# Kernel tuning notes

Hardware: AMD Instinct MI355X
Metric: run time of the kernel (lower is better)

## Reference

```python
import jax, jax.numpy as jnp
import numpy as np

N = 100000
E = 1600000
F = 128
H = 128
EPS = 1e-5
NEG_SLOPE = 0.2


def setup_inputs() -> dict:
    key = jax.random.key(0)
    ks = jax.random.split(key, 24)
    def nrm(k, shape, scale=0.05):
        return jax.random.normal(k, shape, dtype=jnp.float32) * scale
    inp = {
        'x': jax.random.normal(ks[0], (N, F), dtype=jnp.float32),
        'edge_index': jax.random.randint(ks[1], (2, E), 0, N, dtype=jnp.int64),
        # conv 0: F -> H
        'W0': nrm(ks[2], (F, H)), 'asrc0': nrm(ks[3], (H,)), 'adst0': nrm(ks[4], (H,)), 'b0': nrm(ks[5], (H,)),
        # convs 1..4 (middle): H -> H, stacked
        'Wm': nrm(ks[6], (4, H, H)), 'asrcm': nrm(ks[7], (4, H)), 'adstm': nrm(ks[8], (4, H)), 'bm': nrm(ks[9], (4, H)),
        # conv 5 (last): H -> H
        'W5': nrm(ks[10], (H, H)), 'asrc5': nrm(ks[11], (H,)), 'adst5': nrm(ks[12], (H,)), 'b5': nrm(ks[13], (H,)),
        # batchnorm affine params for all 6 layers
        'gammas': jnp.ones((6, H), dtype=jnp.float32), 'betas': jnp.zeros((6, H), dtype=jnp.float32),
        # residual transform F -> H and output layer H -> F
        'Wr': nrm(ks[14], (F, H)), 'br': nrm(ks[15], (H,)),
        'Wo': nrm(ks[16], (H, F)), 'bo': nrm(ks[17], (F,)),
    }
    return inp


def _gat_layer(x, W, a_src, a_dst, b, src, dst):
    # PyG GATConv, heads=1: h = x W; e_ij = LeakyReLU(a_src.h_j + a_dst.h_i)
    # softmax over incoming edges of each destination node, scatter-add aggregate.
    h = x @ W                              # [N, H]
    s = h @ a_src                          # [N]
    d = h @ a_dst                          # [N]
    e = jax.nn.leaky_relu(s[src] + d[dst], NEG_SLOPE)   # [E']
    m = jax.ops.segment_max(e, dst, num_segments=N)      # per-dst max (self-loops guarantee nonempty)
    p = jnp.exp(e - m[dst])
    z = jax.ops.segment_sum(p, dst, num_segments=N)
    alpha = p / z[dst]                     # [E']
    out = jax.ops.segment_sum(alpha[:, None] * h[src], dst, num_segments=N)
    return out + b


def _bn(x, g, beta):
    # BatchNorm1d, training mode (batch statistics, biased variance)
    mu = x.mean(axis=0)
    var = x.var(axis=0)
    return g * (x - mu) * jax.lax.rsqrt(var + EPS) + beta


def reference(x, edge_index, W0, asrc0, adst0, b0, Wm, asrcm, adstm, bm,
              W5, asrc5, adst5, b5, gammas, betas, Wr, br, Wo, bo):
    # add self-loops (PyG GATConv default)
    loops = jnp.arange(N, dtype=edge_index.dtype)
    src = jnp.concatenate([edge_index[0], loops])
    dst = jnp.concatenate([edge_index[1], loops])

    residual = x @ Wr + br
    # first 5 convs: conv -> bn -> relu -> (dropout=identity) -> +residual
    layer_params = [(W0, asrc0, adst0, b0)] + [
        (Wm[i], asrcm[i], adstm[i], bm[i]) for i in range(4)
    ]
    h = x
    for i, (W, a_s, a_d, b) in enumerate(layer_params):
        h = _gat_layer(h, W, a_s, a_d, b, src, dst)
        h = jax.nn.relu(_bn(h, gammas[i], betas[i]))
        h = h + residual
        residual = h
    # last conv -> bn -> out_layer
    h = _gat_layer(h, W5, asrc5, adst5, b5, src, dst)
    h = _bn(h, gammas[5], betas[5])
    return h @ Wo + bo
```

## Files before the change

kernel.cpp:

```cpp
#include <hip/hip_runtime.h>

#define NF 128
#define EPS 1e-5f
#define SLOPE 0.2f

typedef __attribute__((ext_vector_type(8))) short bf16x8;
typedef __attribute__((ext_vector_type(4))) float f32x4;

static __device__ __forceinline__ unsigned short f2bf(float f) {
  unsigned int u = __builtin_bit_cast(unsigned int, f);
  u += 0x7fffu + ((u >> 16) & 1u);
  return (unsigned short)(u >> 16);
}
static __device__ __forceinline__ float bf2f(unsigned short s) {
  return __builtin_bit_cast(float, (unsigned int)s << 16);
}
static __device__ __forceinline__ float bflo(unsigned int u) {
  return __builtin_bit_cast(float, u << 16);
}
static __device__ __forceinline__ float bfhi(unsigned int u) {
  return __builtin_bit_cast(float, u & 0xffff0000u);
}
static __device__ __forceinline__ unsigned int pack2(float a, float b) {
  return (unsigned int)f2bf(a) | ((unsigned int)f2bf(b) << 16);
}


__global__ void k_init_counts(int* counts, int n) {
  int i = blockIdx.x * 256 + threadIdx.x;
  if (i < n) counts[i] = 1;
}

__global__ void k_count(const int* __restrict__ dst, int* __restrict__ counts,
                        int* __restrict__ pos, int e) {
  int i = blockIdx.x * 256 + threadIdx.x;
  if (i < e) pos[i] = atomicAdd(&counts[dst[i]], 1);
}

__global__ void k_scan_part(const int* __restrict__ counts, int* __restrict__ partials, int n) {
  __shared__ int sd[256];
  int base = blockIdx.x * 2048;
  int sum = 0;
  for (int i = threadIdx.x; i < 2048; i += 256) {
    int idx = base + i;
    sum += (idx < n) ? counts[idx] : 0;
  }
  sd[threadIdx.x] = sum;
  __syncthreads();
  for (int s = 128; s > 0; s >>= 1) {
    if (threadIdx.x < s) sd[threadIdx.x] += sd[threadIdx.x + s];
    __syncthreads();
  }
  if (threadIdx.x == 0) partials[blockIdx.x] = sd[0];
}

__global__ void k_scan_mid(int* partials, int nb) {
  if (threadIdx.x == 0 && blockIdx.x == 0) {
    int acc = 0;
    for (int b = 0; b < nb; b++) { int v = partials[b]; partials[b] = acc; acc += v; }
  }
}

__global__ void k_scan_final(const int* __restrict__ counts, const int* __restrict__ partials,
                             int* __restrict__ offsets, int n) {
  __shared__ int sd[256];
  int t = threadIdx.x;
  int base = blockIdx.x * 2048;
  int local[8];
  int sum = 0;
#pragma unroll
  for (int j = 0; j < 8; j++) {
    int idx = base + t * 8 + j;
    int v = (idx < n) ? counts[idx] : 0;
    local[j] = sum;
    sum += v;
  }
  sd[t] = sum;
  __syncthreads();
  for (int st = 1; st < 256; st <<= 1) {
    int v = 0;
    if (t >= st) v = sd[t - st];
    __syncthreads();
    if (t >= st) sd[t] += v;
    __syncthreads();
  }
  int tb = partials[blockIdx.x] + (t > 0 ? sd[t - 1] : 0);
#pragma unroll
  for (int j = 0; j < 8; j++) {
    int idx = base + t * 8 + j;
    if (idx < n) offsets[idx] = tb + local[j];
  }
}

__global__ void k_selfloop(int* __restrict__ offsets, int* __restrict__ csr, int n, int total) {
  int i = blockIdx.x * 256 + threadIdx.x;
  if (i < n) csr[offsets[i]] = i;
  if (i == 0) offsets[n] = total;
}

__global__ void k_fill_pass(const int* __restrict__ src, const int* __restrict__ dst,
                            const int* __restrict__ offsets, const int* __restrict__ pos,
                            int* __restrict__ csr, int e, int lo, int hi) {
  int i = blockIdx.x * 256 + threadIdx.x;
  if (i < e) {
    int d = dst[i];
    if (d >= lo && d < hi) csr[offsets[d] + pos[i]] = src[i];
  }
}


__global__ void k_f32_to_bf16(const float* __restrict__ x, unsigned short* __restrict__ o,
                              int n, int np) {
  int i = blockIdx.x * 256 + threadIdx.x;
  if (i >= np * (NF / 4)) return;
  int row = i >> 5;
  ushort4 ov;
  if (row < n) {
    float4 v = ((const float4*)x)[i];
    ov = make_ushort4(f2bf(v.x), f2bf(v.y), f2bf(v.z), f2bf(v.w));
  } else {
    ov = make_ushort4(0, 0, 0, 0);
  }
  ((ushort4*)o)[i] = ov;
}

__global__ void k_wt(const float* __restrict__ W0, const float* __restrict__ Wm,
                     const float* __restrict__ W5, const float* __restrict__ Wr,
                     const float* __restrict__ Wo, unsigned short* __restrict__ Wt) {
  int idx = blockIdx.x * 256 + threadIdx.x;
  if (idx >= 8 * NF * NF) return;
  int mat = idx >> 14;
  int rem = idx & 16383;
  int r = rem >> 7;
  int k = rem & 127;
  const float* W = (mat == 0) ? W0
                 : (mat <= 4) ? Wm + (size_t)(mat - 1) * NF * NF
                 : (mat == 5) ? W5
                 : (mat == 6) ? Wr : Wo;
  Wt[idx] = f2bf(W[k * NF + r]);
}


template <int MODE>
__global__ __launch_bounds__(256) void k_gemm_mfma(
    const unsigned short* __restrict__ A, const unsigned short* __restrict__ Wt,
    const float* __restrict__ asrc, const float* __restrict__ adst,
    const float* __restrict__ bias, unsigned short* __restrict__ Cb,
    float* __restrict__ Cf, float* __restrict__ sv, float* __restrict__ dv, int n,
    const unsigned short* __restrict__ agg, const unsigned short* __restrict__ res,
    const float* __restrict__ scsh, unsigned short* __restrict__ hout) {
  int w = threadIdx.x >> 6;
  int l = threadIdx.x & 63;
  int lr = l & 15, lh = l >> 4;
  int row0 = blockIdx.x * 128 + w * 32;

  bf16x8 af[2][4];
  if (MODE <= 2) {
    const unsigned short* Ab = A + (size_t)(row0 + lr) * NF + lh * 8;
#pragma unroll
    for (int m = 0; m < 2; m++)
#pragma unroll
      for (int kk = 0; kk < 4; kk++)
        af[m][kk] = *(const bf16x8*)(Ab + m * 16 * NF + kk * 32);
  } else {
#pragma unroll
    for (int kk = 0; kk < 4; kk++) {
      int c0 = lh * 8 + kk * 32;
      float4 scA = *(const float4*)&scsh[c0];
      float4 scB = *(const float4*)&scsh[c0 + 4];
      float4 shA = *(const float4*)&scsh[128 + c0];
      float4 shB = *(const float4*)&scsh[128 + c0 + 4];
#pragma unroll
      for (int m = 0; m < 2; m++) {
        size_t base = (size_t)(row0 + lr + m * 16) * NF + c0;
        uint4 ag = *(const uint4*)(agg + base);
        float v0 = bflo(ag.x) * scA.x + shA.x;
        float v1 = bfhi(ag.x) * scA.y + shA.y;
        float v2 = bflo(ag.y) * scA.z + shA.z;
        float v3 = bfhi(ag.y) * scA.w + shA.w;
        float v4 = bflo(ag.z) * scB.x + shB.x;
        float v5 = bfhi(ag.z) * scB.y + shB.y;
        float v6 = bflo(ag.w) * scB.z + shB.z;
        float v7 = bfhi(ag.w) * scB.w + shB.w;
        if (MODE == 3) {
          uint4 rs = *(const uint4*)(res + base);
          v0 = fmaxf(v0, 0.f) + bflo(rs.x);
          v1 = fmaxf(v1, 0.f) + bfhi(rs.x);
          v2 = fmaxf(v2, 0.f) + bflo(rs.y);
          v3 = fmaxf(v3, 0.f) + bfhi(rs.y);
          v4 = fmaxf(v4, 0.f) + bflo(rs.z);
          v5 = fmaxf(v5, 0.f) + bfhi(rs.z);
          v6 = fmaxf(v6, 0.f) + bflo(rs.w);
          v7 = fmaxf(v7, 0.f) + bfhi(rs.w);
        }
        uint4 hv;
        hv.x = pack2(v0, v1);
        hv.y = pack2(v2, v3);
        hv.z = pack2(v4, v5);
        hv.w = pack2(v6, v7);
        if (MODE == 3) *(uint4*)(hout + base) = hv;
        af[m][kk] = __builtin_bit_cast(bf16x8, hv);
      }
    }
  }

  f32x4 acc[2][8];
#pragma unroll
  for (int m = 0; m < 2; m++)
#pragma unroll
    for (int nn = 0; nn < 8; nn++) acc[m][nn] = (f32x4){0.f, 0.f, 0.f, 0.f};

  const unsigned short* Bb = Wt + (size_t)lr * NF + lh * 8;
#pragma unroll
  for (int kk = 0; kk < 4; kk++) {
    bf16x8 bfr[8];
#pragma unroll
    for (int nn = 0; nn < 8; nn++)
      bfr[nn] = *(const bf16x8*)(Bb + nn * 16 * NF + kk * 32);
#pragma unroll
    for (int m = 0; m < 2; m++)
#pragma unroll
      for (int nn = 0; nn < 8; nn++)
        acc[m][nn] = __builtin_amdgcn_mfma_f32_16x16x32_bf16(af[m][kk], bfr[nn], acc[m][nn], 0, 0, 0);
  }

  if (MODE == 0 || MODE == 3) {
    float as[8], ad[8];
#pragma unroll
    for (int nn = 0; nn < 8; nn++) {
      as[nn] = asrc[nn * 16 + lr];
      ad[nn] = adst[nn * 16 + lr];
    }
#pragma unroll
    for (int m = 0; m < 2; m++) {
#pragma unroll
      for (int r = 0; r < 4; r++) {
        int row = row0 + m * 16 + lh * 4 + r;
        float sp = 0.f, dp = 0.f;
#pragma unroll
        for (int nn = 0; nn < 8; nn++) {
          float v = acc[m][nn][r];
          sp += v * as[nn];
          dp += v * ad[nn];
          Cb[(size_t)row * NF + nn * 16 + lr] = f2bf(v);
        }
#pragma unroll
        for (int mk = 8; mk > 0; mk >>= 1) {
          sp += __shfl_xor(sp, mk);
          dp += __shfl_xor(dp, mk);
        }
        if (lr == 0) { sv[row] = sp; dv[row] = dp; }
      }
    }
  } else if (MODE == 1 || MODE == 4) {
    float bcol[8];
#pragma unroll
    for (int nn = 0; nn < 8; nn++) bcol[nn] = bias[nn * 16 + lr];
#pragma unroll
    for (int m = 0; m < 2; m++)
#pragma unroll
      for (int r = 0; r < 4; r++) {
        int row = row0 + m * 16 + lh * 4 + r;
        if (row < n) {
#pragma unroll
          for (int nn = 0; nn < 8; nn++)
            Cf[(size_t)row * NF + nn * 16 + lr] = acc[m][nn][r] + bcol[nn];
        }
      }
  } else {
    float bcol[8];
#pragma unroll
    for (int nn = 0; nn < 8; nn++) bcol[nn] = bias[nn * 16 + lr];
#pragma unroll
    for (int m = 0; m < 2; m++)
#pragma unroll
      for (int r = 0; r < 4; r++) {
        int row = row0 + m * 16 + lh * 4 + r;
#pragma unroll
        for (int nn = 0; nn < 8; nn++)
          Cb[(size_t)row * NF + nn * 16 + lr] = f2bf(acc[m][nn][r] + bcol[nn]);
      }
  }
}


__global__ __launch_bounds__(256) void k_attn_gather(
    const float* __restrict__ sv, const float* __restrict__ dv,
    const int* __restrict__ offs, const int* __restrict__ csr,
    const unsigned short* __restrict__ hbf, const float* __restrict__ bias,
    unsigned short* __restrict__ aggb, float* __restrict__ pstat, int n) {
  int w = threadIdx.x >> 6, l = threadIdx.x & 63;
  int ll = l & 15, g = l >> 4;
  int node0 = blockIdx.x * 16 + w * 4;
  float ps[8] = {0.f, 0.f, 0.f, 0.f, 0.f, 0.f, 0.f, 0.f};
  float qs[8] = {0.f, 0.f, 0.f, 0.f, 0.f, 0.f, 0.f, 0.f};
  float4 bv0 = *(const float4*)&bias[8 * ll];
  float4 bv1 = *(const float4*)&bias[8 * ll + 4];

  __shared__ uint2 s_pair[4][72];

  for (int ni = 0; ni < 4; ni++) {
    int node = node0 + ni;
    if (node >= n) break;
    int o0 = offs[node], o1 = offs[node + 1];
    int deg = o1 - o0;
    float di = dv[node];
    float a[8] = {0.f, 0.f, 0.f, 0.f, 0.f, 0.f, 0.f, 0.f};

    if (deg <= 64) {
      bool valid = l < deg;
      int srcj = valid ? csr[o0 + l] : 0;
      float ev = valid ? sv[srcj] + di : -1e30f;
      ev = ev >= 0.f ? ev : SLOPE * ev;
      float m = ev;
#pragma unroll
      for (int k2 = 32; k2 > 0; k2 >>= 1) m = fmaxf(m, __shfl_xor(m, k2));
      float pe = valid ? __expf(ev - m) : 0.f;
      float z = pe;
#pragma unroll
      for (int k2 = 32; k2 > 0; k2 >>= 1) z += __shfl_xor(z, k2);
      float wj = pe / z;

      s_pair[w][l] = make_uint2((unsigned)srcj, __builtin_bit_cast(unsigned, wj));
      if (l < 8) s_pair[w][64 + l] = make_uint2(0u, 0u);

      for (int j = g; j < deg; j += 8) {
        uint2 pA = s_pair[w][j];
        uint2 pB = s_pair[w][j + 4];
        int sA = (int)pA.x, sB = (int)pB.x;
        float wA = __builtin_bit_cast(float, pA.y);
        float wB = __builtin_bit_cast(float, pB.y);
        uint4 hA = *(const uint4*)(hbf + (size_t)sA * NF + 8 * ll);
        uint4 hB = *(const uint4*)(hbf + (size_t)sB * NF + 8 * ll);
        a[0] += wA * bflo(hA.x) + wB * bflo(hB.x);
        a[1] += wA * bfhi(hA.x) + wB * bfhi(hB.x);
        a[2] += wA * bflo(hA.y) + wB * bflo(hB.y);
        a[3] += wA * bfhi(hA.y) + wB * bfhi(hB.y);
        a[4] += wA * bflo(hA.z) + wB * bflo(hB.z);
        a[5] += wA * bfhi(hA.z) + wB * bfhi(hB.z);
        a[6] += wA * bflo(hA.w) + wB * bflo(hB.w);
        a[7] += wA * bfhi(hA.w) + wB * bfhi(hB.w);
      }
    } else {
      float m = -1e30f;
      for (int j = o0 + l; j < o1; j += 64) {
        float ev = sv[csr[j]] + di;
        ev = ev >= 0.f ? ev : SLOPE * ev;
        m = fmaxf(m, ev);
      }
#pragma unroll
      for (int k2 = 32; k2 > 0; k2 >>= 1) m = fmaxf(m, __shfl_xor(m, k2));
      float z = 0.f;
      for (int j = o0 + l; j < o1; j += 64) {
        float ev = sv[csr[j]] + di;
        ev = ev >= 0.f ? ev : SLOPE * ev;
        z += __expf(ev - m);
      }
#pragma unroll
      for (int k2 = 32; k2 > 0; k2 >>= 1) z += __shfl_xor(z, k2);
      float inv = 1.f / z;
      for (int t2 = 0; t2 < deg; t2 += 4) {
        int tt = t2 + g;
        if (tt < deg) {
          int sI = csr[o0 + tt];
          float ev = sv[sI] + di;
          ev = ev >= 0.f ? ev : SLOPE * ev;
          float wI = __expf(ev - m) * inv;
          uint4 hv = *(const uint4*)(hbf + (size_t)sI * NF + 8 * ll);
          a[0] += wI * bflo(hv.x);
          a[1] += wI * bfhi(hv.x);
          a[2] += wI * bflo(hv.y);
          a[3] += wI * bfhi(hv.y);
          a[4] += wI * bflo(hv.z);
          a[5] += wI * bfhi(hv.z);
          a[6] += wI * bflo(hv.w);
          a[7] += wI * bfhi(hv.w);
        }
      }
    }
#pragma unroll
    for (int j = 0; j < 8; j++) {
      a[j] += __shfl_xor(a[j], 16);
      a[j] += __shfl_xor(a[j], 32);
    }
    if (g == 0) {
      a[0] += bv0.x; a[1] += bv0.y; a[2] += bv0.z; a[3] += bv0.w;
      a[4] += bv1.x; a[5] += bv1.y; a[6] += bv1.z; a[7] += bv1.w;
      uint4 ov;
      ov.x = pack2(a[0], a[1]);
      ov.y = pack2(a[2], a[3]);
      ov.z = pack2(a[4], a[5]);
      ov.w = pack2(a[6], a[7]);
      *(uint4*)(aggb + (size_t)node * NF + 8 * ll) = ov;
#pragma unroll
      for (int j = 0; j < 8; j++) { ps[j] += a[j]; qs[j] += a[j] * a[j]; }
    }
  }

  __shared__ float red[4][16][17];
  if (g == 0) {
#pragma unroll
    for (int j = 0; j < 8; j++) {
      red[w][ll][j] = ps[j];
      red[w][ll][8 + j] = qs[j];
    }
  }
  __syncthreads();
  int t = threadIdx.x;
  int c = t & 127, kind = t >> 7;
  int li = c >> 3, sj = (c & 7) + 8 * kind;
  float v = red[0][li][sj] + red[1][li][sj] + red[2][li][sj] + red[3][li][sj];
  atomicAdd(&pstat[(blockIdx.x & 63) * 256 + t], v);
}


__global__ void k_bnfinal(float* __restrict__ pstat, const float* __restrict__ gamma,
                          const float* __restrict__ beta, float* __restrict__ scsh,
                          float ninv) {
  __shared__ float tot[256];
  int t = threadIdx.x;
  float v = 0.f;
  for (int s2 = 0; s2 < 64; s2++) {
    v += pstat[s2 * 256 + t];
    pstat[s2 * 256 + t] = 0.f;
  }
  tot[t] = v;
  __syncthreads();
  if (t < 128) {
    float mu = tot[t] * ninv;
    float var = tot[128 + t] * ninv - mu * mu;
    float sc = gamma[t] * rsqrtf(var + EPS);
    scsh[t] = sc;
    scsh[128 + t] = beta[t] - mu * sc;
  }
}


extern "C" void kernel_launch(void* const* d_in, const int* in_sizes, int n_in,
                              void* d_out, int out_size, void* d_ws, size_t ws_size,
                              hipStream_t stream) {
  (void)n_in; (void)out_size; (void)ws_size;
  const float* x     = (const float*)d_in[0];
  const int*   ei    = (const int*)d_in[1];
  const float* W0    = (const float*)d_in[2];
  const float* asrc0 = (const float*)d_in[3];
  const float* adst0 = (const float*)d_in[4];
  const float* b0    = (const float*)d_in[5];
  const float* Wm    = (const float*)d_in[6];
  const float* asrcm = (const float*)d_in[7];
  const float* adstm = (const float*)d_in[8];
  const float* bm    = (const float*)d_in[9];
  const float* W5    = (const float*)d_in[10];
  const float* asrc5 = (const float*)d_in[11];
  const float* adst5 = (const float*)d_in[12];
  const float* b5    = (const float*)d_in[13];
  const float* gammas= (const float*)d_in[14];
  const float* betas = (const float*)d_in[15];
  const float* Wr    = (const float*)d_in[16];
  const float* br    = (const float*)d_in[17];
  const float* Wo    = (const float*)d_in[18];
  const float* bo    = (const float*)d_in[19];

  const int n = in_sizes[0] / NF;
  const int np = (n + 127) & ~127;
  const int e = in_sizes[1] / 2;
  const int tot = e + n;
  const int* srcp = ei;
  const int* dstp = ei + e;

  char* w = (char*)d_ws;
  auto carve = [&](size_t bytes) {
    char* p = w;
    w += (bytes + 255) & ~(size_t)255;
    return p;
  };
  unsigned short* h_bf    = (unsigned short*)carve((size_t)np * NF * 2);
  unsigned short* hlin_bf = (unsigned short*)carve((size_t)np * NF * 2);
  unsigned short* res_bf  = (unsigned short*)carve((size_t)np * NF * 2);
  unsigned short* agg_bf  = (unsigned short*)carve((size_t)np * NF * 2);
  unsigned short* Wt      = (unsigned short*)carve((size_t)8 * NF * NF * 2);
  float* sv      = (float*)carve((size_t)np * 4);
  float* dv      = (float*)carve((size_t)np * 4);
  int*   csr     = (int*)carve((size_t)tot * 4);
  int*   offsets = (int*)carve((size_t)(n + 1) * 4);
  int*   counts  = (int*)carve((size_t)n * 4);
  int*   pos     = (int*)carve((size_t)e * 4);
  int*   partials= (int*)carve(64 * 4);
  float* pstat   = (float*)carve(64 * 256 * 4);
  float* scsh    = (float*)carve(256 * 4);

  int nb = (n + 2047) / 2048;

  k_wt<<<(8 * NF * NF + 255) / 256, 256, 0, stream>>>(W0, Wm, W5, Wr, Wo, Wt);
  k_f32_to_bf16<<<(np * (NF / 4) + 255) / 256, 256, 0, stream>>>(x, h_bf, n, np);

  k_init_counts<<<(n + 255) / 256, 256, 0, stream>>>(counts, n);
  k_count<<<(e + 255) / 256, 256, 0, stream>>>(dstp, counts, pos, e);
  k_scan_part<<<nb, 256, 0, stream>>>(counts, partials, n);
  k_scan_mid<<<1, 64, 0, stream>>>(partials, nb);
  k_scan_final<<<nb, 256, 0, stream>>>(counts, partials, offsets, n);
  k_selfloop<<<(n + 255) / 256, 256, 0, stream>>>(offsets, csr, n, tot);
  {
    const int NPASS = 8;
    int step = (n + NPASS - 1) / NPASS;
    for (int p = 0; p < NPASS; p++) {
      int lo = p * step;
      int hi = min(n, lo + step);
      k_fill_pass<<<(e + 255) / 256, 256, 0, stream>>>(srcp, dstp, offsets, pos, csr, e, lo, hi);
    }
  }

  hipMemsetAsync(pstat, 0, 64 * 256 * 4, stream);

  int gemm_grid = np / 128;

  k_gemm_mfma<2><<<gemm_grid, 256, 0, stream>>>(h_bf, Wt + 6 * NF * NF, nullptr, nullptr,
                                                br, res_bf, nullptr, nullptr, nullptr, n,
                                                nullptr, nullptr, nullptr, nullptr);

  for (int L = 0; L < 6; L++) {
    const float *als, *ald, *bl;
    if (L == 0)      { als = asrc0; ald = adst0; bl = b0; }
    else if (L <= 4) { als = asrcm + (L - 1) * NF; ald = adstm + (L - 1) * NF; bl = bm + (L - 1) * NF; }
    else             { als = asrc5; ald = adst5; bl = b5; }

    if (L == 0) {
      k_gemm_mfma<0><<<gemm_grid, 256, 0, stream>>>(h_bf, Wt, als, ald, nullptr, hlin_bf,
                                                    nullptr, sv, dv, n,
                                                    nullptr, nullptr, nullptr, nullptr);
    } else {
      const unsigned short* resb = (L == 1) ? res_bf : h_bf;
      k_gemm_mfma<3><<<gemm_grid, 256, 0, stream>>>(nullptr, Wt + (size_t)L * NF * NF,
                                                    als, ald, nullptr, hlin_bf, nullptr, sv, dv, n,
                                                    agg_bf, resb, scsh, h_bf);
    }

    k_attn_gather<<<(n + 15) / 16, 256, 0, stream>>>(sv, dv, offsets, csr, hlin_bf, bl,
                                                     agg_bf, pstat, n);
    k_bnfinal<<<1, 256, 0, stream>>>(pstat, gammas + L * NF, betas + L * NF, scsh, 1.0f / n);
  }

  k_gemm_mfma<4><<<gemm_grid, 256, 0, stream>>>(nullptr, Wt + 7 * NF * NF, nullptr, nullptr,
                                                bo, nullptr, (float*)d_out, nullptr, nullptr, n,
                                                agg_bf, nullptr, scsh, nullptr);
}
```

Before: 890.5 us.

## Split attention into alpha pass and feature-sliced gather over column-sliced h

```diff
diff --git a/kernel.cpp b/kernel.cpp
--- a/kernel.cpp
+++ b/kernel.cpp
@@ -11,9 +11,6 @@
   unsigned int u = __builtin_bit_cast(unsigned int, f);
   u += 0x7fffu + ((u >> 16) & 1u);
   return (unsigned short)(u >> 16);
-}
-static __device__ __forceinline__ float bf2f(unsigned short s) {
-  return __builtin_bit_cast(float, (unsigned int)s << 16);
 }
 static __device__ __forceinline__ float bflo(unsigned int u) {
   return __builtin_bit_cast(float, u << 16);
@@ -153,6 +150,7 @@
   int l = threadIdx.x & 63;
   int lr = l & 15, lh = l >> 4;
   int row0 = blockIdx.x * 128 + w * 32;
+  size_t sstr = (size_t)gridDim.x * 128 * 16;
 
   bf16x8 af[2][4];
   if (MODE <= 2) {
@@ -242,7 +240,7 @@
           float v = acc[m][nn][r];
           sp += v * as[nn];
           dp += v * ad[nn];
-          Cb[(size_t)row * NF + nn * 16 + lr] = f2bf(v);
+          Cb[(size_t)nn * sstr + (size_t)row * 16 + lr] = f2bf(v);
         }
 #pragma unroll
         for (int mk = 8; mk > 0; mk >>= 1) {
@@ -284,29 +282,18 @@
 }
 
 
-__global__ __launch_bounds__(256) void k_attn_gather(
+__global__ __launch_bounds__(256) void k_alpha(
     const float* __restrict__ sv, const float* __restrict__ dv,
     const int* __restrict__ offs, const int* __restrict__ csr,
-    const unsigned short* __restrict__ hbf, const float* __restrict__ bias,
-    unsigned short* __restrict__ aggb, float* __restrict__ pstat, int n) {
+    unsigned int* __restrict__ packed, int n) {
   int w = threadIdx.x >> 6, l = threadIdx.x & 63;
-  int ll = l & 15, g = l >> 4;
   int node0 = blockIdx.x * 16 + w * 4;
-  float ps[8] = {0.f, 0.f, 0.f, 0.f, 0.f, 0.f, 0.f, 0.f};
-  float qs[8] = {0.f, 0.f, 0.f, 0.f, 0.f, 0.f, 0.f, 0.f};
-  float4 bv0 = *(const float4*)&bias[8 * ll];
-  float4 bv1 = *(const float4*)&bias[8 * ll + 4];
-
-  __shared__ uint2 s_pair[4][72];
-
   for (int ni = 0; ni < 4; ni++) {
     int node = node0 + ni;
     if (node >= n) break;
     int o0 = offs[node], o1 = offs[node + 1];
     int deg = o1 - o0;
     float di = dv[node];
-    float a[8] = {0.f, 0.f, 0.f, 0.f, 0.f, 0.f, 0.f, 0.f};
-
     if (deg <= 64) {
       bool valid = l < deg;
       int srcj = valid ? csr[o0 + l] : 0;
@@ -320,26 +307,9 @@
 #pragma unroll
       for (int k2 = 32; k2 > 0; k2 >>= 1) z += __shfl_xor(z, k2);
       float wj = pe / z;
-
-      s_pair[w][l] = make_uint2((unsigned)srcj, __builtin_bit_cast(unsigned, wj));
-      if (l < 8) s_pair[w][64 + l] = make_uint2(0u, 0u);
-
-      for (int j = g; j < deg; j += 8) {
-        uint2 pA = s_pair[w][j];
-        uint2 pB = s_pair[w][j + 4];
-        int sA = (int)pA.x, sB = (int)pB.x;
-        float wA = __builtin_bit_cast(float, pA.y);
-        float wB = __builtin_bit_cast(float, pB.y);
-        uint4 hA = *(const uint4*)(hbf + (size_t)sA * NF + 8 * ll);
-        uint4 hB = *(const uint4*)(hbf + (size_t)sB * NF + 8 * ll);
-        a[0] += wA * bflo(hA.x) + wB * bflo(hB.x);
-        a[1] += wA * bfhi(hA.x) + wB * bfhi(hB.x);
-        a[2] += wA * bflo(hA.y) + wB * bflo(hB.y);
-        a[3] += wA * bfhi(hA.y) + wB * bfhi(hB.y);
-        a[4] += wA * bflo(hA.z) + wB * bflo(hB.z);
-        a[5] += wA * bfhi(hA.z) + wB * bfhi(hB.z);
-        a[6] += wA * bflo(hA.w) + wB * bflo(hB.w);
-        a[7] += wA * bfhi(hA.w) + wB * bfhi(hB.w);
+      if (valid) {
+        unsigned q = (unsigned)(wj * 32767.f + 0.5f);
+        packed[o0 + l] = ((unsigned)srcj << 15) | q;
       }
     } else {
       float m = -1e30f;
@@ -359,58 +329,84 @@
 #pragma unroll
       for (int k2 = 32; k2 > 0; k2 >>= 1) z += __shfl_xor(z, k2);
       float inv = 1.f / z;
-      for (int t2 = 0; t2 < deg; t2 += 4) {
-        int tt = t2 + g;
-        if (tt < deg) {
-          int sI = csr[o0 + tt];
-          float ev = sv[sI] + di;
-          ev = ev >= 0.f ? ev : SLOPE * ev;
-          float wI = __expf(ev - m) * inv;
-          uint4 hv = *(const uint4*)(hbf + (size_t)sI * NF + 8 * ll);
-          a[0] += wI * bflo(hv.x);
-          a[1] += wI * bfhi(hv.x);
-          a[2] += wI * bflo(hv.y);
-          a[3] += wI * bfhi(hv.y);
-          a[4] += wI * bflo(hv.z);
-          a[5] += wI * bfhi(hv.z);
-          a[6] += wI * bflo(hv.w);
-          a[7] += wI * bfhi(hv.w);
-        }
-      }
-    }
-#pragma unroll
-    for (int j = 0; j < 8; j++) {
-      a[j] += __shfl_xor(a[j], 16);
-      a[j] += __shfl_xor(a[j], 32);
-    }
-    if (g == 0) {
-      a[0] += bv0.x; a[1] += bv0.y; a[2] += bv0.z; a[3] += bv0.w;
-      a[4] += bv1.x; a[5] += bv1.y; a[6] += bv1.z; a[7] += bv1.w;
-      uint4 ov;
-      ov.x = pack2(a[0], a[1]);
-      ov.y = pack2(a[2], a[3]);
-      ov.z = pack2(a[4], a[5]);
-      ov.w = pack2(a[6], a[7]);
-      *(uint4*)(aggb + (size_t)node * NF + 8 * ll) = ov;
-#pragma unroll
-      for (int j = 0; j < 8; j++) { ps[j] += a[j]; qs[j] += a[j] * a[j]; }
-    }
-  }
-
-  __shared__ float red[4][16][17];
-  if (g == 0) {
-#pragma unroll
-    for (int j = 0; j < 8; j++) {
-      red[w][ll][j] = ps[j];
-      red[w][ll][8 + j] = qs[j];
-    }
+      for (int j = o0 + l; j < o1; j += 64) {
+        int sI = csr[j];
+        float ev = sv[sI] + di;
+        ev = ev >= 0.f ? ev : SLOPE * ev;
+        float wj = __expf(ev - m) * inv;
+        unsigned q = (unsigned)(wj * 32767.f + 0.5f);
+        packed[j] = ((unsigned)sI << 15) | q;
+      }
+    }
+  }
+}
+
+
+__global__ __launch_bounds__(256) void k_gather_slice(
+    const unsigned int* __restrict__ packed, const int* __restrict__ offs,
+    const unsigned short* __restrict__ hs, const float* __restrict__ bias,
+    unsigned short* __restrict__ aggb, float* __restrict__ pstat, int n, int np) {
+  int slice = blockIdx.x & 7;
+  int chunk = blockIdx.x >> 3;
+  int th = threadIdx.x;
+  int w2 = th >> 6, l = th & 63;
+  int h2 = l >> 5, lh2 = l & 31;
+  int e = lh2 >> 2, c = lh2 & 3;
+  const unsigned short* hsl = hs + (size_t)slice * np * 16 + c * 4;
+  float4 bv = *(const float4*)&bias[slice * 16 + c * 4];
+  float ps0 = 0.f, ps1 = 0.f, ps2 = 0.f, ps3 = 0.f;
+  float qs0 = 0.f, qs1 = 0.f, qs2 = 0.f, qs3 = 0.f;
+
+  for (int r = 0; r < 8; r++) {
+    int node = chunk * 64 + r * 8 + w2 * 2 + h2;
+    float a0 = 0.f, a1 = 0.f, a2 = 0.f, a3 = 0.f;
+    if (node < n) {
+      int o0 = offs[node], o1 = offs[node + 1];
+      for (int j = o0 + e; j < o1; j += 8) {
+        unsigned u = packed[j];
+        float al = (float)(u & 32767u) * (1.f / 32767.f);
+        uint2 hv = *(const uint2*)(hsl + (size_t)(u >> 15) * 16);
+        a0 += al * bflo(hv.x);
+        a1 += al * bfhi(hv.x);
+        a2 += al * bflo(hv.y);
+        a3 += al * bfhi(hv.y);
+      }
+    }
+#pragma unroll
+    for (int mk = 4; mk <= 16; mk <<= 1) {
+      a0 += __shfl_xor(a0, mk);
+      a1 += __shfl_xor(a1, mk);
+      a2 += __shfl_xor(a2, mk);
+      a3 += __shfl_xor(a3, mk);
+    }
+    if (e == 0 && node < n) {
+      a0 += bv.x; a1 += bv.y; a2 += bv.z; a3 += bv.w;
+      *(uint2*)(aggb + (size_t)node * NF + slice * 16 + c * 4) =
+          make_uint2(pack2(a0, a1), pack2(a2, a3));
+      ps0 += a0; qs0 += a0 * a0;
+      ps1 += a1; qs1 += a1 * a1;
+      ps2 += a2; qs2 += a2 * a2;
+      ps3 += a3; qs3 += a3 * a3;
+    }
+  }
+
+  __shared__ float sred[8][4][4], qred[8][4][4];
+  if (e == 0) {
+    int who = w2 * 2 + h2;
+    sred[who][c][0] = ps0; sred[who][c][1] = ps1;
+    sred[who][c][2] = ps2; sred[who][c][3] = ps3;
+    qred[who][c][0] = qs0; qred[who][c][1] = qs1;
+    qred[who][c][2] = qs2; qred[who][c][3] = qs3;
   }
   __syncthreads();
-  int t = threadIdx.x;
-  int c = t & 127, kind = t >> 7;
-  int li = c >> 3, sj = (c & 7) + 8 * kind;
-  float v = red[0][li][sj] + red[1][li][sj] + red[2][li][sj] + red[3][li][sj];
-  atomicAdd(&pstat[(blockIdx.x & 63) * 256 + t], v);
+  if (th < 32) {
+    int kind = th >> 4, lc = th & 15;
+    float s = 0.f;
+#pragma unroll
+    for (int i = 0; i < 8; i++)
+      s += kind ? qred[i][lc >> 2][lc & 3] : sred[i][lc >> 2][lc & 3];
+    atomicAdd(&pstat[(size_t)((blockIdx.x >> 3) & 63) * 256 + kind * 128 + slice * 16 + lc], s);
+  }
 }
 
 
@@ -475,13 +471,14 @@
     return p;
   };
   unsigned short* h_bf    = (unsigned short*)carve((size_t)np * NF * 2);
-  unsigned short* hlin_bf = (unsigned short*)carve((size_t)np * NF * 2);
+  unsigned short* hs      = (unsigned short*)carve((size_t)np * NF * 2);
   unsigned short* res_bf  = (unsigned short*)carve((size_t)np * NF * 2);
   unsigned short* agg_bf  = (unsigned short*)carve((size_t)np * NF * 2);
   unsigned short* Wt      = (unsigned short*)carve((size_t)8 * NF * NF * 2);
   float* sv      = (float*)carve((size_t)np * 4);
   float* dv      = (float*)carve((size_t)np * 4);
   int*   csr     = (int*)carve((size_t)tot * 4);
+  unsigned int* packed = (unsigned int*)carve((size_t)tot * 4);
   int*   offsets = (int*)carve((size_t)(n + 1) * 4);
   int*   counts  = (int*)carve((size_t)n * 4);
   int*   pos     = (int*)carve((size_t)e * 4);
@@ -513,6 +510,7 @@
   hipMemsetAsync(pstat, 0, 64 * 256 * 4, stream);
 
   int gemm_grid = np / 128;
+  int gs_grid = ((n + 63) / 64) * 8;
 
   k_gemm_mfma<2><<<gemm_grid, 256, 0, stream>>>(h_bf, Wt + 6 * NF * NF, nullptr, nullptr,
                                                 br, res_bf, nullptr, nullptr, nullptr, n,
@@ -525,18 +523,18 @@
     else             { als = asrc5; ald = adst5; bl = b5; }
 
     if (L == 0) {
-      k_gemm_mfma<0><<<gemm_grid, 256, 0, stream>>>(h_bf, Wt, als, ald, nullptr, hlin_bf,
+      k_gemm_mfma<0><<<gemm_grid, 256, 0, stream>>>(h_bf, Wt, als, ald, nullptr, hs,
                                                     nullptr, sv, dv, n,
                                                     nullptr, nullptr, nullptr, nullptr);
     } else {
       const unsigned short* resb = (L == 1) ? res_bf : h_bf;
       k_gemm_mfma<3><<<gemm_grid, 256, 0, stream>>>(nullptr, Wt + (size_t)L * NF * NF,
-                                                    als, ald, nullptr, hlin_bf, nullptr, sv, dv, n,
+                                                    als, ald, nullptr, hs, nullptr, sv, dv, n,
                                                     agg_bf, resb, scsh, h_bf);
     }
 
-    k_attn_gather<<<(n + 15) / 16, 256, 0, stream>>>(sv, dv, offsets, csr, hlin_bf, bl,
-                                                     agg_bf, pstat, n);
+    k_alpha<<<(n + 15) / 16, 256, 0, stream>>>(sv, dv, offsets, csr, packed, n);
+    k_gather_slice<<<gs_grid, 256, 0, stream>>>(packed, offsets, hs, bl, agg_bf, pstat, n, np);
     k_bnfinal<<<1, 256, 0, stream>>>(pstat, gammas + L * NF, betas + L * NF, scsh, 1.0f / n);
   }
 
```

Measured after the change: 1.351 ms. 51.7% more time.

## Build CSR with per-node atomic cursors and skip unused residual store in last layer

Applied to the files above, without the earlier changes.

```diff
diff --git a/kernel.cpp b/kernel.cpp
--- a/kernel.cpp
+++ b/kernel.cpp
@@ -12,9 +12,6 @@
   u += 0x7fffu + ((u >> 16) & 1u);
   return (unsigned short)(u >> 16);
 }
-static __device__ __forceinline__ float bf2f(unsigned short s) {
-  return __builtin_bit_cast(float, (unsigned int)s << 16);
-}
 static __device__ __forceinline__ float bflo(unsigned int u) {
   return __builtin_bit_cast(float, u << 16);
 }
@@ -31,10 +28,9 @@
   if (i < n) counts[i] = 1;
 }
 
-__global__ void k_count(const int* __restrict__ dst, int* __restrict__ counts,
-                        int* __restrict__ pos, int e) {
+__global__ void k_count(const int* __restrict__ dst, int* __restrict__ counts, int e) {
   int i = blockIdx.x * 256 + threadIdx.x;
-  if (i < e) pos[i] = atomicAdd(&counts[dst[i]], 1);
+  if (i < e) atomicAdd(&counts[dst[i]], 1);
 }
 
 __global__ void k_scan_part(const int* __restrict__ counts, int* __restrict__ partials, int n) {
@@ -92,19 +88,27 @@
   }
 }
 
-__global__ void k_selfloop(int* __restrict__ offsets, int* __restrict__ csr, int n, int total) {
+__global__ void k_selfloop(int* __restrict__ offsets, int* __restrict__ cursor,
+                           int* __restrict__ csr, int n, int total) {
   int i = blockIdx.x * 256 + threadIdx.x;
-  if (i < n) csr[offsets[i]] = i;
+  if (i < n) {
+    int o = offsets[i];
+    csr[o] = i;
+    cursor[i] = o + 1;
+  }
   if (i == 0) offsets[n] = total;
 }
 
 __global__ void k_fill_pass(const int* __restrict__ src, const int* __restrict__ dst,
-                            const int* __restrict__ offsets, const int* __restrict__ pos,
-                            int* __restrict__ csr, int e, int lo, int hi) {
+                            int* __restrict__ cursor, int* __restrict__ csr,
+                            int e, int lo, int hi) {
   int i = blockIdx.x * 256 + threadIdx.x;
   if (i < e) {
     int d = dst[i];
-    if (d >= lo && d < hi) csr[offsets[d] + pos[i]] = src[i];
+    if (d >= lo && d < hi) {
+      int p = atomicAdd(&cursor[d], 1);
+      csr[p] = src[i];
+    }
   }
 }
 
@@ -198,7 +202,7 @@
         hv.y = pack2(v2, v3);
         hv.z = pack2(v4, v5);
         hv.w = pack2(v6, v7);
-        if (MODE == 3) *(uint4*)(hout + base) = hv;
+        if (MODE == 3 && hout) *(uint4*)(hout + base) = hv;
         af[m][kk] = __builtin_bit_cast(bf16x8, hv);
       }
     }
@@ -484,7 +488,7 @@
   int*   csr     = (int*)carve((size_t)tot * 4);
   int*   offsets = (int*)carve((size_t)(n + 1) * 4);
   int*   counts  = (int*)carve((size_t)n * 4);
-  int*   pos     = (int*)carve((size_t)e * 4);
+  int*   cursor  = (int*)carve((size_t)n * 4);
   int*   partials= (int*)carve(64 * 4);
   float* pstat   = (float*)carve(64 * 256 * 4);
   float* scsh    = (float*)carve(256 * 4);
@@ -495,18 +499,18 @@
   k_f32_to_bf16<<<(np * (NF / 4) + 255) / 256, 256, 0, stream>>>(x, h_bf, n, np);
 
   k_init_counts<<<(n + 255) / 256, 256, 0, stream>>>(counts, n);
-  k_count<<<(e + 255) / 256, 256, 0, stream>>>(dstp, counts, pos, e);
+  k_count<<<(e + 255) / 256, 256, 0, stream>>>(dstp, counts, e);
   k_scan_part<<<nb, 256, 0, stream>>>(counts, partials, n);
   k_scan_mid<<<1, 64, 0, stream>>>(partials, nb);
   k_scan_final<<<nb, 256, 0, stream>>>(counts, partials, offsets, n);
-  k_selfloop<<<(n + 255) / 256, 256, 0, stream>>>(offsets, csr, n, tot);
+  k_selfloop<<<(n + 255) / 256, 256, 0, stream>>>(offsets, cursor, csr, n, tot);
   {
-    const int NPASS = 8;
+    const int NPASS = 4;
     int step = (n + NPASS - 1) / NPASS;
     for (int p = 0; p < NPASS; p++) {
       int lo = p * step;
       int hi = min(n, lo + step);
-      k_fill_pass<<<(e + 255) / 256, 256, 0, stream>>>(srcp, dstp, offsets, pos, csr, e, lo, hi);
+      k_fill_pass<<<(e + 255) / 256, 256, 0, stream>>>(srcp, dstp, cursor, csr, e, lo, hi);
     }
   }
 
@@ -530,9 +534,10 @@
                                                     nullptr, nullptr, nullptr, nullptr);
     } else {
       const unsigned short* resb = (L == 1) ? res_bf : h_bf;
+      unsigned short* houtp = (L < 5) ? h_bf : nullptr;
       k_gemm_mfma<3><<<gemm_grid, 256, 0, stream>>>(nullptr, Wt + (size_t)L * NF * NF,
                                                     als, ald, nullptr, hlin_bf, nullptr, sv, dv, n,
-                                                    agg_bf, resb, scsh, h_bf);
+                                                    agg_bf, resb, scsh, houtp);
     }
 
     k_attn_gather<<<(n + 15) / 16, 256, 0, stream>>>(sv, dv, offsets, csr, hlin_bf, bl,
```

Result: slower. 943.6 us (+6.0%).

## Split attention gather across column halves, single-pass CSR fill, skip unused h write

Applied to the files above, without the earlier changes.

```diff
diff --git a/kernel.cpp b/kernel.cpp
--- a/kernel.cpp
+++ b/kernel.cpp
@@ -11,9 +11,6 @@
   unsigned int u = __builtin_bit_cast(unsigned int, f);
   u += 0x7fffu + ((u >> 16) & 1u);
   return (unsigned short)(u >> 16);
-}
-static __device__ __forceinline__ float bf2f(unsigned short s) {
-  return __builtin_bit_cast(float, (unsigned int)s << 16);
 }
 static __device__ __forceinline__ float bflo(unsigned int u) {
   return __builtin_bit_cast(float, u << 16);
@@ -98,14 +95,11 @@
   if (i == 0) offsets[n] = total;
 }
 
-__global__ void k_fill_pass(const int* __restrict__ src, const int* __restrict__ dst,
-                            const int* __restrict__ offsets, const int* __restrict__ pos,
-                            int* __restrict__ csr, int e, int lo, int hi) {
+__global__ void k_fill(const int* __restrict__ src, const int* __restrict__ dst,
+                       const int* __restrict__ offsets, const int* __restrict__ pos,
+                       int* __restrict__ csr, int e) {
   int i = blockIdx.x * 256 + threadIdx.x;
-  if (i < e) {
-    int d = dst[i];
-    if (d >= lo && d < hi) csr[offsets[d] + pos[i]] = src[i];
-  }
+  if (i < e) csr[offsets[dst[i]] + pos[i]] = src[i];
 }
 
 
@@ -198,7 +192,7 @@
         hv.y = pack2(v2, v3);
         hv.z = pack2(v4, v5);
         hv.w = pack2(v6, v7);
-        if (MODE == 3) *(uint4*)(hout + base) = hv;
+        if (MODE == 3 && hout) *(uint4*)(hout + base) = hv;
         af[m][kk] = __builtin_bit_cast(bf16x8, hv);
       }
     }
@@ -290,14 +284,18 @@
     const unsigned short* __restrict__ hbf, const float* __restrict__ bias,
     unsigned short* __restrict__ aggb, float* __restrict__ pstat, int n) {
   int w = threadIdx.x >> 6, l = threadIdx.x & 63;
-  int ll = l & 15, g = l >> 4;
-  int node0 = blockIdx.x * 16 + w * 4;
+  int half = blockIdx.x & 1;
+  int chunk = blockIdx.x >> 1;
+  int e8 = l >> 3, c8 = l & 7;
+  int colbase = half * 64 + c8 * 8;
+  int node0 = chunk * 16 + w * 4;
   float ps[8] = {0.f, 0.f, 0.f, 0.f, 0.f, 0.f, 0.f, 0.f};
   float qs[8] = {0.f, 0.f, 0.f, 0.f, 0.f, 0.f, 0.f, 0.f};
-  float4 bv0 = *(const float4*)&bias[8 * ll];
-  float4 bv1 = *(const float4*)&bias[8 * ll + 4];
-
-  __shared__ uint2 s_pair[4][72];
+  float4 bv0 = *(const float4*)&bias[colbase];
+  float4 bv1 = *(const float4*)&bias[colbase + 4];
+
+  __shared__ uint2 s_pair[4][80];
+  if (l < 16) s_pair[w][64 + l] = make_uint2(0u, 0u);
 
   for (int ni = 0; ni < 4; ni++) {
     int node = node0 + ni;
@@ -322,16 +320,14 @@
       float wj = pe / z;
 
       s_pair[w][l] = make_uint2((unsigned)srcj, __builtin_bit_cast(unsigned, wj));
-      if (l < 8) s_pair[w][64 + l] = make_uint2(0u, 0u);
-
-      for (int j = g; j < deg; j += 8) {
+
+      for (int j = e8; j < deg; j += 16) {
         uint2 pA = s_pair[w][j];
-        uint2 pB = s_pair[w][j + 4];
-        int sA = (int)pA.x, sB = (int)pB.x;
+        uint2 pB = s_pair[w][j + 8];
         float wA = __builtin_bit_cast(float, pA.y);
         float wB = __builtin_bit_cast(float, pB.y);
-        uint4 hA = *(const uint4*)(hbf + (size_t)sA * NF + 8 * ll);
-        uint4 hB = *(const uint4*)(hbf + (size_t)sB * NF + 8 * ll);
+        uint4 hA = *(const uint4*)(hbf + (size_t)pA.x * NF + colbase);
+        uint4 hB = *(const uint4*)(hbf + (size_t)pB.x * NF + colbase);
         a[0] += wA * bflo(hA.x) + wB * bflo(hB.x);
         a[1] += wA * bfhi(hA.x) + wB * bfhi(hB.x);
         a[2] += wA * bflo(hA.y) + wB * bflo(hB.y);
@@ -359,31 +355,29 @@
 #pragma unroll
       for (int k2 = 32; k2 > 0; k2 >>= 1) z += __shfl_xor(z, k2);
       float inv = 1.f / z;
-      for (int t2 = 0; t2 < deg; t2 += 4) {
-        int tt = t2 + g;
-        if (tt < deg) {
-          int sI = csr[o0 + tt];
-          float ev = sv[sI] + di;
-          ev = ev >= 0.f ? ev : SLOPE * ev;
-          float wI = __expf(ev - m) * inv;
-          uint4 hv = *(const uint4*)(hbf + (size_t)sI * NF + 8 * ll);
-          a[0] += wI * bflo(hv.x);
-          a[1] += wI * bfhi(hv.x);
-          a[2] += wI * bflo(hv.y);
-          a[3] += wI * bfhi(hv.y);
-          a[4] += wI * bflo(hv.z);
-          a[5] += wI * bfhi(hv.z);
-          a[6] += wI * bflo(hv.w);
-          a[7] += wI * bfhi(hv.w);
-        }
+      for (int tt = o0 + e8; tt < o1; tt += 8) {
+        int sI = csr[tt];
+        float ev = sv[sI] + di;
+        ev = ev >= 0.f ? ev : SLOPE * ev;
+        float wI = __expf(ev - m) * inv;
+        uint4 hv = *(const uint4*)(hbf + (size_t)sI * NF + colbase);
+        a[0] += wI * bflo(hv.x);
+        a[1] += wI * bfhi(hv.x);
+        a[2] += wI * bflo(hv.y);
+        a[3] += wI * bfhi(hv.y);
+        a[4] += wI * bflo(hv.z);
+        a[5] += wI * bfhi(hv.z);
+        a[6] += wI * bflo(hv.w);
+        a[7] += wI * bfhi(hv.w);
       }
     }
 #pragma unroll
     for (int j = 0; j < 8; j++) {
+      a[j] += __shfl_xor(a[j], 8);
       a[j] += __shfl_xor(a[j], 16);
       a[j] += __shfl_xor(a[j], 32);
     }
-    if (g == 0) {
+    if (e8 == 0) {
       a[0] += bv0.x; a[1] += bv0.y; a[2] += bv0.z; a[3] += bv0.w;
       a[4] += bv1.x; a[5] += bv1.y; a[6] += bv1.z; a[7] += bv1.w;
       uint4 ov;
@@ -391,26 +385,29 @@
       ov.y = pack2(a[2], a[3]);
       ov.z = pack2(a[4], a[5]);
       ov.w = pack2(a[6], a[7]);
-      *(uint4*)(aggb + (size_t)node * NF + 8 * ll) = ov;
+      *(uint4*)(aggb + (size_t)node * NF + colbase) = ov;
 #pragma unroll
       for (int j = 0; j < 8; j++) { ps[j] += a[j]; qs[j] += a[j] * a[j]; }
     }
   }
 
-  __shared__ float red[4][16][17];
-  if (g == 0) {
+  __shared__ float red[4][8][17];
+  if (e8 == 0) {
 #pragma unroll
     for (int j = 0; j < 8; j++) {
-      red[w][ll][j] = ps[j];
-      red[w][ll][8 + j] = qs[j];
+      red[w][c8][j] = ps[j];
+      red[w][c8][8 + j] = qs[j];
     }
   }
   __syncthreads();
   int t = threadIdx.x;
-  int c = t & 127, kind = t >> 7;
-  int li = c >> 3, sj = (c & 7) + 8 * kind;
-  float v = red[0][li][sj] + red[1][li][sj] + red[2][li][sj] + red[3][li][sj];
-  atomicAdd(&pstat[(blockIdx.x & 63) * 256 + t], v);
+  if (t < 128) {
+    int kind = t >> 6;
+    int cc = t & 63;
+    int ci = cc >> 3, ck = (cc & 7) + 8 * kind;
+    float v = red[0][ci][ck] + red[1][ci][ck] + red[2][ci][ck] + red[3][ci][ck];
+    atomicAdd(&pstat[((blockIdx.x >> 1) & 63) * 256 + kind * 128 + half * 64 + cc], v);
+  }
 }
 
 
@@ -500,19 +497,12 @@
   k_scan_mid<<<1, 64, 0, stream>>>(partials, nb);
   k_scan_final<<<nb, 256, 0, stream>>>(counts, partials, offsets, n);
   k_selfloop<<<(n + 255) / 256, 256, 0, stream>>>(offsets, csr, n, tot);
-  {
-    const int NPASS = 8;
-    int step = (n + NPASS - 1) / NPASS;
-    for (int p = 0; p < NPASS; p++) {
-      int lo = p * step;
-      int hi = min(n, lo + step);
-      k_fill_pass<<<(e + 255) / 256, 256, 0, stream>>>(srcp, dstp, offsets, pos, csr, e, lo, hi);
-    }
-  }
+  k_fill<<<(e + 255) / 256, 256, 0, stream>>>(srcp, dstp, offsets, pos, csr, e);
 
   hipMemsetAsync(pstat, 0, 64 * 256 * 4, stream);
 
   int gemm_grid = np / 128;
+  int gather_grid = 2 * ((n + 15) / 16);
 
   k_gemm_mfma<2><<<gemm_grid, 256, 0, stream>>>(h_bf, Wt + 6 * NF * NF, nullptr, nullptr,
                                                 br, res_bf, nullptr, nullptr, nullptr, n,
@@ -530,13 +520,14 @@
                                                     nullptr, nullptr, nullptr, nullptr);
     } else {
       const unsigned short* resb = (L == 1) ? res_bf : h_bf;
+      unsigned short* houtp = (L < 5) ? h_bf : nullptr;
       k_gemm_mfma<3><<<gemm_grid, 256, 0, stream>>>(nullptr, Wt + (size_t)L * NF * NF,
                                                     als, ald, nullptr, hlin_bf, nullptr, sv, dv, n,
-                                                    agg_bf, resb, scsh, h_bf);
-    }
-
-    k_attn_gather<<<(n + 15) / 16, 256, 0, stream>>>(sv, dv, offsets, csr, hlin_bf, bl,
-                                                     agg_bf, pstat, n);
+                                                    agg_bf, resb, scsh, houtp);
+    }
+
+    k_attn_gather<<<gather_grid, 256, 0, stream>>>(sv, dv, offsets, csr, hlin_bf, bl,
+                                                   agg_bf, pstat, n);
     k_bnfinal<<<1, 256, 0, stream>>>(pstat, gammas + L * NF, betas + L * NF, scsh, 1.0f / n);
   }
 
```

Result: slower. 1.162 ms (+30.4%).
